# Kernel optimization log

Hardware: AMD Instinct MI355X
Metric: run time of the kernel (lower is better)

## Reference

```python
import jax, jax.numpy as jnp
import numpy as np

LN_EPS = 1e-12

def setup_inputs() -> dict:
    key = jax.random.key(0)
    k1, k2 = jax.random.split(key)
    B, S, H = 32, 2048, 1024
    input_tensor = jax.random.normal(k1, (B, S, H), dtype=jnp.float32)
    # learned params
    complex_weight = jax.random.normal(k2, (1, S // 2 + 1, H, 2), dtype=jnp.float32) * 0.02
    ln_gamma = jnp.ones((H,), dtype=jnp.float32)
    ln_beta = jnp.zeros((H,), dtype=jnp.float32)
    return {"input_tensor": input_tensor, "complex_weight": complex_weight,
            "ln_gamma": ln_gamma, "ln_beta": ln_beta}

def reference(input_tensor, complex_weight, ln_gamma, ln_beta):
    B, S, H = input_tensor.shape
    # FFT filter: rfft along seq, complex elementwise multiply, irfft
    x = jnp.fft.rfft(input_tensor, axis=1, norm='ortho')            # [B, S//2+1, H] complex64
    weight = complex_weight[..., 0] + 1j * complex_weight[..., 1]   # [1, S//2+1, H]
    x = x * weight
    seq_fft = jnp.fft.irfft(x, n=S, axis=1, norm='ortho')           # [B, S, H] real
    # dropout is identity in eval mode
    h = seq_fft + input_tensor
    # LayerNorm over last dim, eps=1e-12, biased variance (torch semantics)
    mean = jnp.mean(h, axis=-1, keepdims=True)
    var = jnp.mean(jnp.square(h - mean), axis=-1, keepdims=True)
    normed = (h - mean) * jax.lax.rsqrt(var + LN_EPS)
    return normed * ln_gamma + ln_beta
```

## Files before the change

kernel.cpp:

```cpp
#include <hip/hip_runtime.h>
#include <math.h>


#define PI_F 3.14159265358979323846f
#define SW(c) ((c) ^ (((c) >> 4) & 15))

__device__ __forceinline__ float2 cadd(float2 a, float2 b){ return make_float2(a.x+b.x, a.y+b.y); }
__device__ __forceinline__ float2 csub(float2 a, float2 b){ return make_float2(a.x-b.x, a.y-b.y); }
__device__ __forceinline__ float2 cmul(float2 a, float2 b){ return make_float2(a.x*b.x - a.y*b.y, a.x*b.y + a.y*b.x); }

template<int L>
__device__ __forceinline__ void fwd_stage(float2* A, int j){
  constexpr int half = L >> 1;
  const float ang0 = -PI_F / (float)L;
  #pragma unroll
  for (int r = 0; r < 4; ++r){
    int g    = j + (r << 7);
    int blk  = g / half;
    int joff = g - blk * half;
    int i0   = blk * (2 * L) + joff;
    float2 u0 = A[SW(i0)];
    float2 u1 = A[SW(i0 + half)];
    float2 u2 = A[SW(i0 + L)];
    float2 u3 = A[SW(i0 + L + half)];
    float sn, cs; __sincosf(ang0 * (float)joff, &sn, &cs);
    float2 w1 = make_float2(cs, sn);
    float2 t0  = cadd(u0, u2);
    float2 d02 = csub(u0, u2);
    float2 t1  = cadd(u1, u3);
    float2 d13 = csub(u1, u3);
    float2 t2  = cmul(d02, w1);
    float2 tm  = cmul(d13, w1);
    float2 t3  = make_float2(tm.y, -tm.x);
    float2 w2  = cmul(w1, w1);
    A[SW(i0)]            = cadd(t0, t1);
    A[SW(i0 + half)]     = cmul(csub(t0, t1), w2);
    A[SW(i0 + L)]        = cadd(t2, t3);
    A[SW(i0 + L + half)] = cmul(csub(t2, t3), w2);
  }
}

template<int l>
__device__ __forceinline__ void inv_stage(float2* A, int j){
  const float angB = PI_F / (float)(2 * l);
  #pragma unroll
  for (int r = 0; r < 4; ++r){
    int g    = j + (r << 7);
    int blk  = g / l;
    int joff = g - blk * l;
    int base = blk * (4 * l);
    int i0 = base + joff;
    float2 u0 = A[SW(i0)];
    float2 u1 = A[SW(i0 + l)];
    float2 u2 = A[SW(i0 + 2*l)];
    float2 u3 = A[SW(i0 + 3*l)];
    float sn, cs; __sincosf(angB * (float)joff, &sn, &cs);
    float2 wB = make_float2(cs, sn);
    float2 w  = cmul(wB, wB);
    float2 a1 = cmul(u1, w);
    float2 b0 = cadd(u0, a1), b1 = csub(u0, a1);
    float2 a3 = cmul(u3, w);
    float2 b2 = cadd(u2, a3), b3 = csub(u2, a3);
    float2 t2 = cmul(b2, wB);
    float2 c0 = cadd(b0, t2), c2 = csub(b0, t2);
    float2 iwB = make_float2(-wB.y, wB.x);
    float2 t3 = cmul(b3, iwB);
    float2 c1 = cadd(b1, t3), c3 = csub(b1, t3);
    A[SW(i0)]       = c0;
    A[SW(i0 + l)]   = c1;
    A[SW(i0 + 2*l)] = c2;
    A[SW(i0 + 3*l)] = c3;
  }
}

__device__ __forceinline__ float2 fetchW(const float2* __restrict__ wT,
                                         const float2* __restrict__ cw,
                                         int useT, int h, int k){
  if (useT) return wT[(size_t)h * 1025 + k];
  float2 w = cw[(size_t)k * 1024 + h];
  const float inv = 1.0f / 2048.0f;
  return make_float2((w.x + 1.0f) * inv, w.y * inv);
}

__global__ void prep_w_kernel(const float2* __restrict__ cw, float2* __restrict__ wT){
  __shared__ float2 tile[32][33];
  int k0 = blockIdx.x * 32, h0 = blockIdx.y * 32;
  int tx = threadIdx.x, ty = threadIdx.y;
  #pragma unroll
  for (int r = 0; r < 4; ++r){
    int k = k0 + ty + 8 * r;
    if (k < 1025) tile[ty + 8*r][tx] = cw[(size_t)k * 1024 + (h0 + tx)];
  }
  __syncthreads();
  const float inv = 1.0f / 2048.0f;
  #pragma unroll
  for (int r = 0; r < 4; ++r){
    int h = h0 + ty + 8 * r;
    int k = k0 + tx;
    if (k < 1025){
      float2 w = tile[tx][ty + 8*r];
      wT[(size_t)h * 1025 + k] = make_float2((w.x + 1.0f) * inv, w.y * inv);
    }
  }
}

__global__ __launch_bounds__(512) void fft_filter_kernel(
    const float2* __restrict__ x,
    const float2* __restrict__ cw,
    const float2* __restrict__ wT,
    int useT,
    float2* __restrict__ out){
  __shared__ float2 lds[4][2048];
  const int t  = threadIdx.x;
  const int bx = blockIdx.x;
  const int b  = bx >> 7;
  const int pg = bx & 127;
  const int f  = t >> 7;
  const int j  = t & 127;
  float2* A = lds[f];

  {
    const int p4 = t & 3, srow = t >> 2;
    const size_t base = ((size_t)b * 2048) * 512 + (size_t)(pg * 4 + p4);
    #pragma unroll
    for (int it = 0; it < 16; ++it){
      int s = srow + (it << 7);
      lds[p4][SW(s)] = x[base + (size_t)s * 512];
    }
  }
  __syncthreads();

  fwd_stage<1024>(A, j); __syncthreads();
  fwd_stage<256>(A, j);  __syncthreads();
  fwd_stage<64>(A, j);   __syncthreads();
  fwd_stage<16>(A, j);   __syncthreads();
  fwd_stage<4>(A, j);    __syncthreads();
  #pragma unroll
  for (int r = 0; r < 8; ++r){
    int m = j + (r << 7);
    int ia = SW(2*m), ib = SW(2*m + 1);
    float2 u = A[ia], v = A[ib];
    A[ia] = cadd(u, v);
    A[ib] = csub(u, v);
  }
  __syncthreads();

  {
    const int hA = (pg << 3) + (f << 1);
    if (j == 0){
      float2 z0 = A[0];
      float2 wa = fetchW(wT, cw, useT, hA, 0);
      float2 wb = fetchW(wT, cw, useT, hA + 1, 0);
      A[0] = make_float2(z0.x * wa.x, z0.y * wb.x);
      int p1 = SW(1);
      float2 zn = A[p1];
      wa = fetchW(wT, cw, useT, hA, 1024);
      wb = fetchW(wT, cw, useT, hA + 1, 1024);
      A[p1] = make_float2(zn.x * wa.x, zn.y * wb.x);
    }
    #pragma unroll
    for (int r = 0; r < 8; ++r){
      int k = 1 + j + (r << 7);
      if (k < 1024){
        int kr = 2048 - k;
        int p1 = SW((int)(__brev((unsigned)k) >> 21));
        int p2 = SW((int)(__brev((unsigned)kr) >> 21));
        float2 Z1 = A[p1], Z2 = A[p2];
        float2 Xa = make_float2(0.5f*(Z1.x + Z2.x), 0.5f*(Z1.y - Z2.y));
        float2 Xb = make_float2(0.5f*(Z1.y + Z2.y), 0.5f*(Z2.x - Z1.x));
        float2 wa = fetchW(wT, cw, useT, hA, k);
        float2 wb = fetchW(wT, cw, useT, hA + 1, k);
        float2 Ya = cmul(Xa, wa);
        float2 Yb = cmul(Xb, wb);
        A[p1] = make_float2(Ya.x - Yb.y, Ya.y + Yb.x);
        A[p2] = make_float2(Ya.x + Yb.y, Yb.x - Ya.y);
      }
    }
  }
  __syncthreads();

  #pragma unroll
  for (int r = 0; r < 8; ++r){
    int m = j + (r << 7);
    int ia = SW(2*m), ib = SW(2*m + 1);
    float2 u = A[ia], v = A[ib];
    A[ia] = cadd(u, v);
    A[ib] = csub(u, v);
  }
  __syncthreads();
  inv_stage<2>(A, j);   __syncthreads();
  inv_stage<8>(A, j);   __syncthreads();
  inv_stage<32>(A, j);  __syncthreads();
  inv_stage<128>(A, j); __syncthreads();
  inv_stage<512>(A, j); __syncthreads();

  {
    const int p4 = t & 3, srow = t >> 2;
    const size_t base = ((size_t)b * 2048) * 512 + (size_t)(pg * 4 + p4);
    #pragma unroll
    for (int it = 0; it < 16; ++it){
      int s = srow + (it << 7);
      out[base + (size_t)s * 512] = lds[p4][SW(s)];
    }
  }
}

__global__ __launch_bounds__(256) void ln_kernel(float* __restrict__ io,
                                                 const float* __restrict__ gma,
                                                 const float* __restrict__ bta){
  const int row = blockIdx.x;
  const int t = threadIdx.x;
  float4* r4 = (float4*)io + (size_t)row * 256;
  float4 v = r4[t];
  float s1 = v.x + v.y + v.z + v.w;
  float s2 = v.x*v.x + v.y*v.y + v.z*v.z + v.w*v.w;
  #pragma unroll
  for (int off = 32; off > 0; off >>= 1){
    s1 += __shfl_down(s1, off);
    s2 += __shfl_down(s2, off);
  }
  __shared__ float red[8];
  __shared__ float mr[2];
  const int wid = t >> 6, lane = t & 63;
  if (lane == 0){ red[wid] = s1; red[4 + wid] = s2; }
  __syncthreads();
  if (t == 0){
    float ts1 = red[0] + red[1] + red[2] + red[3];
    float ts2 = red[4] + red[5] + red[6] + red[7];
    float mean = ts1 * (1.0f / 1024.0f);
    float var  = ts2 * (1.0f / 1024.0f) - mean * mean;
    mr[0] = mean;
    mr[1] = rsqrtf(fmaxf(var, 0.0f) + 1e-12f);
  }
  __syncthreads();
  const float mean = mr[0], rstd = mr[1];
  const float4 gv = ((const float4*)gma)[t];
  const float4 bv = ((const float4*)bta)[t];
  float4 o;
  o.x = (v.x - mean) * rstd * gv.x + bv.x;
  o.y = (v.y - mean) * rstd * gv.y + bv.y;
  o.z = (v.z - mean) * rstd * gv.z + bv.z;
  o.w = (v.w - mean) * rstd * gv.w + bv.w;
  r4[t] = o;
}

extern "C" void kernel_launch(void* const* d_in, const int* in_sizes, int n_in,
                              void* d_out, int out_size, void* d_ws, size_t ws_size,
                              hipStream_t stream){
  const float2* x2  = (const float2*)d_in[0];
  const float2* cw2 = (const float2*)d_in[1];
  const float*  gma = (const float*)d_in[2];
  const float*  bta = (const float*)d_in[3];
  float2* out2 = (float2*)d_out;
  float*  outf = (float*)d_out;

  const int Bn = in_sizes[0] / (2048 * 1024);

  const size_t needW = (size_t)1025 * 1024 * sizeof(float2);
  const int useT = (ws_size >= needW) ? 1 : 0;
  float2* wT = (float2*)d_ws;

  if (useT){
    hipLaunchKernelGGL(prep_w_kernel, dim3(33, 32), dim3(32, 8), 0, stream, cw2, wT);
  }
  hipLaunchKernelGGL(fft_filter_kernel, dim3(Bn * 128), dim3(512), 0, stream,
                     x2, cw2, wT, useT, out2);
  hipLaunchKernelGGL(ln_kernel, dim3(Bn * 2048), dim3(256), 0, stream,
                     outf, gma, bta);
}
```

Measured before the change: 891.6 us.

## Replace radix-4 LDS FFT stages with register radix-16 plus shuffle stages

Result: slower. 1.635 ms (+83.4%).

```diff
diff --git a/kernel.cpp b/kernel.cpp
--- a/kernel.cpp
+++ b/kernel.cpp
@@ -2,75 +2,61 @@
 #include <math.h>
 
 
-#define PI_F 3.14159265358979323846f
-#define SW(c) ((c) ^ (((c) >> 4) & 15))
+#define C8f  0.70710678118654752f
+#define SIN1 0.38268343236508977f
+#define COS1 0.92387953251128674f
+
+#define SW4(i) ((i) ^ ((((i) >> 8) & 7) << 3))
+
+static constexpr int BR4[16] = {0,8,4,12,2,10,6,14,1,9,5,13,3,11,7,15};
 
 __device__ __forceinline__ float2 cadd(float2 a, float2 b){ return make_float2(a.x+b.x, a.y+b.y); }
 __device__ __forceinline__ float2 csub(float2 a, float2 b){ return make_float2(a.x-b.x, a.y-b.y); }
 __device__ __forceinline__ float2 cmul(float2 a, float2 b){ return make_float2(a.x*b.x - a.y*b.y, a.x*b.y + a.y*b.x); }
 
-template<int L>
-__device__ __forceinline__ void fwd_stage(float2* A, int j){
-  constexpr int half = L >> 1;
-  const float ang0 = -PI_F / (float)L;
-  #pragma unroll
-  for (int r = 0; r < 4; ++r){
-    int g    = j + (r << 7);
-    int blk  = g / half;
-    int joff = g - blk * half;
-    int i0   = blk * (2 * L) + joff;
-    float2 u0 = A[SW(i0)];
-    float2 u1 = A[SW(i0 + half)];
-    float2 u2 = A[SW(i0 + L)];
-    float2 u3 = A[SW(i0 + L + half)];
-    float sn, cs; __sincosf(ang0 * (float)joff, &sn, &cs);
-    float2 w1 = make_float2(cs, sn);
-    float2 t0  = cadd(u0, u2);
-    float2 d02 = csub(u0, u2);
-    float2 t1  = cadd(u1, u3);
-    float2 d13 = csub(u1, u3);
-    float2 t2  = cmul(d02, w1);
-    float2 tm  = cmul(d13, w1);
-    float2 t3  = make_float2(tm.y, -tm.x);
-    float2 w2  = cmul(w1, w1);
-    A[SW(i0)]            = cadd(t0, t1);
-    A[SW(i0 + half)]     = cmul(csub(t0, t1), w2);
-    A[SW(i0 + L)]        = cadd(t2, t3);
-    A[SW(i0 + L + half)] = cmul(csub(t2, t3), w2);
-  }
-}
-
-template<int l>
-__device__ __forceinline__ void inv_stage(float2* A, int j){
-  const float angB = PI_F / (float)(2 * l);
-  #pragma unroll
-  for (int r = 0; r < 4; ++r){
-    int g    = j + (r << 7);
-    int blk  = g / l;
-    int joff = g - blk * l;
-    int base = blk * (4 * l);
-    int i0 = base + joff;
-    float2 u0 = A[SW(i0)];
-    float2 u1 = A[SW(i0 + l)];
-    float2 u2 = A[SW(i0 + 2*l)];
-    float2 u3 = A[SW(i0 + 3*l)];
-    float sn, cs; __sincosf(angB * (float)joff, &sn, &cs);
-    float2 wB = make_float2(cs, sn);
-    float2 w  = cmul(wB, wB);
-    float2 a1 = cmul(u1, w);
-    float2 b0 = cadd(u0, a1), b1 = csub(u0, a1);
-    float2 a3 = cmul(u3, w);
-    float2 b2 = cadd(u2, a3), b3 = csub(u2, a3);
-    float2 t2 = cmul(b2, wB);
-    float2 c0 = cadd(b0, t2), c2 = csub(b0, t2);
-    float2 iwB = make_float2(-wB.y, wB.x);
-    float2 t3 = cmul(b3, iwB);
-    float2 c1 = cadd(b1, t3), c3 = csub(b1, t3);
-    A[SW(i0)]       = c0;
-    A[SW(i0 + l)]   = c1;
-    A[SW(i0 + 2*l)] = c2;
-    A[SW(i0 + 3*l)] = c3;
-  }
+__device__ __forceinline__ void dft16_fwd(float2* r){
+  const float WR[8] = {1.f,  COS1,  C8f,  SIN1, 0.f, -SIN1, -C8f, -COS1};
+  const float WI[8] = {0.f, -SIN1, -C8f, -COS1, -1.f, -COS1, -C8f, -SIN1};
+  #pragma unroll
+  for (int m = 0; m < 8; ++m){
+    float2 u = r[m], v = r[m+8];
+    r[m] = cadd(u, v);
+    float2 d = csub(u, v);
+    r[m+8] = make_float2(d.x*WR[m] - d.y*WI[m], d.x*WI[m] + d.y*WR[m]);
+  }
+  #pragma unroll
+  for (int h = 0; h < 16; h += 8){
+    #pragma unroll
+    for (int m = 0; m < 4; ++m){
+      float2 u = r[h+m], v = r[h+m+4];
+      r[h+m] = cadd(u, v);
+      float2 d = csub(u, v);
+      r[h+m+4] = make_float2(d.x*WR[2*m] - d.y*WI[2*m], d.x*WI[2*m] + d.y*WR[2*m]);
+    }
+  }
+  #pragma unroll
+  for (int h = 0; h < 16; h += 4){
+    { float2 u=r[h],   v=r[h+2]; r[h]  =cadd(u,v); r[h+2]=csub(u,v); }
+    { float2 u=r[h+1], v=r[h+3]; float2 d=csub(u,v); r[h+1]=cadd(u,v); r[h+3]=make_float2(d.y, -d.x); }
+  }
+  #pragma unroll
+  for (int h = 0; h < 16; h += 2){
+    float2 u=r[h], v=r[h+1]; r[h]=cadd(u,v); r[h+1]=csub(u,v);
+  }
+}
+
+__device__ __forceinline__ void twiddle_apply(float2* r, float2 step){
+  float2 tw = step;
+  #pragma unroll
+  for (int k = 1; k < 16; ++k){
+    int p = BR4[k];
+    r[p] = cmul(r[p], tw);
+    if (k < 15) tw = cmul(tw, step);
+  }
+}
+
+__device__ __forceinline__ float2 shflx(float2 v, int m){
+  return make_float2(__shfl_xor(v.x, m, 64), __shfl_xor(v.y, m, 64));
 }
 
 __device__ __forceinline__ float2 fetchW(const float2* __restrict__ wT,
@@ -104,7 +90,7 @@
   }
 }
 
-__global__ __launch_bounds__(512) void fft_filter_kernel(
+__global__ __launch_bounds__(512, 4) void fft_filter_kernel(
     const float2* __restrict__ x,
     const float2* __restrict__ cw,
     const float2* __restrict__ wT,
@@ -125,74 +111,130 @@
     #pragma unroll
     for (int it = 0; it < 16; ++it){
       int s = srow + (it << 7);
-      lds[p4][SW(s)] = x[base + (size_t)s * 512];
-    }
-  }
-  __syncthreads();
-
-  fwd_stage<1024>(A, j); __syncthreads();
-  fwd_stage<256>(A, j);  __syncthreads();
-  fwd_stage<64>(A, j);   __syncthreads();
-  fwd_stage<16>(A, j);   __syncthreads();
-  fwd_stage<4>(A, j);    __syncthreads();
-  #pragma unroll
-  for (int r = 0; r < 8; ++r){
-    int m = j + (r << 7);
-    int ia = SW(2*m), ib = SW(2*m + 1);
-    float2 u = A[ia], v = A[ib];
-    A[ia] = cadd(u, v);
-    A[ib] = csub(u, v);
-  }
-  __syncthreads();
-
-  {
-    const int hA = (pg << 3) + (f << 1);
-    if (j == 0){
-      float2 z0 = A[0];
+      lds[p4][SW4(s)] = x[base + (size_t)s * 512];
+    }
+  }
+  __syncthreads();
+
+  float2 r[16];
+  const int k1 = j >> 3, bb = j & 7;
+  const int rb = ((bb & 1) << 2) | (bb & 2) | ((bb & 4) >> 2);
+
+  const float2 w8c = make_float2((bb & 1) ? ((bb & 2) ? -C8f : C8f) : ((bb & 2) ? 0.f : 1.f),
+                                 (bb & 1) ? -C8f : ((bb & 2) ? -1.f : 0.f));
+  const float2 w4c = (bb & 1) ? make_float2(0.f, -1.f) : make_float2(1.f, 0.f);
+  const bool h4 = (bb & 4), h2 = (bb & 2), h1 = (bb & 1);
+
+  float sn, cs;
+  __sincosf(-6.2831853071795864769f * (float)j * (1.0f / 2048.0f), &sn, &cs);
+  const float2 stepJ = make_float2(cs, sn);
+  __sincosf(-6.2831853071795864769f * (float)bb * (1.0f / 128.0f), &sn, &cs);
+  const float2 stepB = make_float2(cs, sn);
+
+  #pragma unroll
+  for (int n1 = 0; n1 < 16; ++n1) r[n1] = A[SW4(128 * n1 + j)];
+  dft16_fwd(r);
+  twiddle_apply(r, stepJ);
+  __syncthreads();
+  #pragma unroll
+  for (int p = 0; p < 16; ++p){
+    int kk1 = BR4[p];
+    A[128 * kk1 + (j ^ ((kk1 & 1) << 3))] = r[p];
+  }
+  __syncthreads();
+
+  #pragma unroll
+  for (int a = 0; a < 16; ++a)
+    r[a] = A[128 * k1 + (((a << 3) + bb) ^ ((k1 & 1) << 3))];
+  dft16_fwd(r);
+  twiddle_apply(r, stepB);
+
+  #pragma unroll
+  for (int p = 0; p < 16; ++p){
+    float2 z = r[p];
+    float2 tt = shflx(z, 4);
+    float2 a1 = h4 ? csub(tt, z) : cadd(z, tt);
+    z = h4 ? cmul(a1, w8c) : a1;
+    tt = shflx(z, 2);
+    a1 = h2 ? csub(tt, z) : cadd(z, tt);
+    z = h2 ? cmul(a1, w4c) : a1;
+    tt = shflx(z, 1);
+    r[p] = h1 ? csub(tt, z) : cadd(z, tt);
+  }
+  __syncthreads();
+  #pragma unroll
+  for (int p = 0; p < 16; ++p){
+    int c = BR4[p];
+    int k = k1 + (c << 4) + (rb << 8);
+    A[SW4(k)] = r[p];
+  }
+  __syncthreads();
+
+  const int hA = (pg << 3) + (f << 1);
+  #pragma unroll
+  for (int q = 0; q < 16; ++q){
+    int kk = (q << 7) + j;
+    float2 V;
+    if (kk == 0){
+      float2 X0 = A[SW4(0)];
       float2 wa = fetchW(wT, cw, useT, hA, 0);
       float2 wb = fetchW(wT, cw, useT, hA + 1, 0);
-      A[0] = make_float2(z0.x * wa.x, z0.y * wb.x);
-      int p1 = SW(1);
-      float2 zn = A[p1];
-      wa = fetchW(wT, cw, useT, hA, 1024);
-      wb = fetchW(wT, cw, useT, hA + 1, 1024);
-      A[p1] = make_float2(zn.x * wa.x, zn.y * wb.x);
-    }
-    #pragma unroll
-    for (int r = 0; r < 8; ++r){
-      int k = 1 + j + (r << 7);
-      if (k < 1024){
-        int kr = 2048 - k;
-        int p1 = SW((int)(__brev((unsigned)k) >> 21));
-        int p2 = SW((int)(__brev((unsigned)kr) >> 21));
-        float2 Z1 = A[p1], Z2 = A[p2];
-        float2 Xa = make_float2(0.5f*(Z1.x + Z2.x), 0.5f*(Z1.y - Z2.y));
-        float2 Xb = make_float2(0.5f*(Z1.y + Z2.y), 0.5f*(Z2.x - Z1.x));
-        float2 wa = fetchW(wT, cw, useT, hA, k);
-        float2 wb = fetchW(wT, cw, useT, hA + 1, k);
-        float2 Ya = cmul(Xa, wa);
-        float2 Yb = cmul(Xb, wb);
-        A[p1] = make_float2(Ya.x - Yb.y, Ya.y + Yb.x);
-        A[p2] = make_float2(Ya.x + Yb.y, Yb.x - Ya.y);
-      }
-    }
-  }
-  __syncthreads();
-
-  #pragma unroll
-  for (int r = 0; r < 8; ++r){
-    int m = j + (r << 7);
-    int ia = SW(2*m), ib = SW(2*m + 1);
-    float2 u = A[ia], v = A[ib];
-    A[ia] = cadd(u, v);
-    A[ib] = csub(u, v);
-  }
-  __syncthreads();
-  inv_stage<2>(A, j);   __syncthreads();
-  inv_stage<8>(A, j);   __syncthreads();
-  inv_stage<32>(A, j);  __syncthreads();
-  inv_stage<128>(A, j); __syncthreads();
-  inv_stage<512>(A, j); __syncthreads();
+      V = make_float2(X0.x * wa.x, X0.y * wb.x);
+    } else if (kk == 1024){
+      float2 Xn = A[SW4(1024)];
+      float2 wa = fetchW(wT, cw, useT, hA, 1024);
+      float2 wb = fetchW(wT, cw, useT, hA + 1, 1024);
+      V = make_float2(Xn.x * wa.x, Xn.y * wb.x);
+    } else {
+      int k = (kk < 1024) ? kk : 2048 - kk;
+      float2 Z1 = A[SW4(k)];
+      float2 Z2 = A[SW4(2048 - k)];
+      float2 wa = fetchW(wT, cw, useT, hA, k);
+      float2 wb = fetchW(wT, cw, useT, hA + 1, k);
+      float2 Xa = make_float2(0.5f*(Z1.x + Z2.x), 0.5f*(Z1.y - Z2.y));
+      float2 Xb = make_float2(0.5f*(Z1.y + Z2.y), 0.5f*(Z2.x - Z1.x));
+      float2 Ya = cmul(Xa, wa);
+      float2 Yb = cmul(Xb, wb);
+      V = (kk < 1024) ? make_float2(Ya.x - Yb.y, Ya.y + Yb.x)
+                      : make_float2(Ya.x + Yb.y, Yb.x - Ya.y);
+    }
+    r[q] = make_float2(V.x, -V.y);
+  }
+
+  dft16_fwd(r);
+  twiddle_apply(r, stepJ);
+  __syncthreads();
+  #pragma unroll
+  for (int p = 0; p < 16; ++p){
+    int s1 = BR4[p];
+    A[128 * s1 + (j ^ ((s1 & 1) << 3))] = r[p];
+  }
+  __syncthreads();
+  #pragma unroll
+  for (int a = 0; a < 16; ++a)
+    r[a] = A[128 * k1 + (((a << 3) + bb) ^ ((k1 & 1) << 3))];
+  dft16_fwd(r);
+  twiddle_apply(r, stepB);
+  #pragma unroll
+  for (int p = 0; p < 16; ++p){
+    float2 z = r[p];
+    float2 tt = shflx(z, 4);
+    float2 a1 = h4 ? csub(tt, z) : cadd(z, tt);
+    z = h4 ? cmul(a1, w8c) : a1;
+    tt = shflx(z, 2);
+    a1 = h2 ? csub(tt, z) : cadd(z, tt);
+    z = h2 ? cmul(a1, w4c) : a1;
+    tt = shflx(z, 1);
+    r[p] = h1 ? csub(tt, z) : cadd(z, tt);
+  }
+  __syncthreads();
+  #pragma unroll
+  for (int p = 0; p < 16; ++p){
+    int g = BR4[p];
+    int s = k1 + (g << 4) + (rb << 8);
+    A[SW4(s)] = make_float2(r[p].x, -r[p].y);
+  }
+  __syncthreads();
 
   {
     const int p4 = t & 3, srow = t >> 2;
@@ -200,7 +242,7 @@
     #pragma unroll
     for (int it = 0; it < 16; ++it){
       int s = srow + (it << 7);
-      out[base + (size_t)s * 512] = lds[p4][SW(s)];
+      out[base + (size_t)s * 512] = lds[p4][SW4(s)];
     }
   }
 }
@@ -208,40 +250,38 @@
 __global__ __launch_bounds__(256) void ln_kernel(float* __restrict__ io,
                                                  const float* __restrict__ gma,
                                                  const float* __restrict__ bta){
-  const int row = blockIdx.x;
   const int t = threadIdx.x;
-  float4* r4 = (float4*)io + (size_t)row * 256;
-  float4 v = r4[t];
-  float s1 = v.x + v.y + v.z + v.w;
-  float s2 = v.x*v.x + v.y*v.y + v.z*v.z + v.w*v.w;
-  #pragma unroll
-  for (int off = 32; off > 0; off >>= 1){
-    s1 += __shfl_down(s1, off);
-    s2 += __shfl_down(s2, off);
-  }
-  __shared__ float red[8];
-  __shared__ float mr[2];
-  const int wid = t >> 6, lane = t & 63;
-  if (lane == 0){ red[wid] = s1; red[4 + wid] = s2; }
-  __syncthreads();
-  if (t == 0){
-    float ts1 = red[0] + red[1] + red[2] + red[3];
-    float ts2 = red[4] + red[5] + red[6] + red[7];
-    float mean = ts1 * (1.0f / 1024.0f);
-    float var  = ts2 * (1.0f / 1024.0f) - mean * mean;
-    mr[0] = mean;
-    mr[1] = rsqrtf(fmaxf(var, 0.0f) + 1e-12f);
-  }
-  __syncthreads();
-  const float mean = mr[0], rstd = mr[1];
-  const float4 gv = ((const float4*)gma)[t];
-  const float4 bv = ((const float4*)bta)[t];
-  float4 o;
-  o.x = (v.x - mean) * rstd * gv.x + bv.x;
-  o.y = (v.y - mean) * rstd * gv.y + bv.y;
-  o.z = (v.z - mean) * rstd * gv.z + bv.z;
-  o.w = (v.w - mean) * rstd * gv.w + bv.w;
-  r4[t] = o;
+  const int lane = t & 63;
+  const size_t row = (size_t)blockIdx.x * 4 + (t >> 6);
+  float4* r4 = (float4*)io + row * 256;
+  const float4* g4 = (const float4*)gma;
+  const float4* b4 = (const float4*)bta;
+  float4 v[4];
+  #pragma unroll
+  for (int i = 0; i < 4; ++i) v[i] = r4[lane + 64 * i];
+  float s1 = 0.f, s2 = 0.f;
+  #pragma unroll
+  for (int i = 0; i < 4; ++i){
+    s1 += v[i].x + v[i].y + v[i].z + v[i].w;
+    s2 += v[i].x*v[i].x + v[i].y*v[i].y + v[i].z*v[i].z + v[i].w*v[i].w;
+  }
+  #pragma unroll
+  for (int m = 32; m >= 1; m >>= 1){
+    s1 += __shfl_xor(s1, m, 64);
+    s2 += __shfl_xor(s2, m, 64);
+  }
+  const float mean = s1 * (1.0f / 1024.0f);
+  const float var  = s2 * (1.0f / 1024.0f) - mean * mean;
+  const float rstd = rsqrtf(fmaxf(var, 0.0f) + 1e-12f);
+  #pragma unroll
+  for (int i = 0; i < 4; ++i){
+    float4 gv = g4[lane + 64 * i], bv = b4[lane + 64 * i], o;
+    o.x = (v[i].x - mean) * rstd * gv.x + bv.x;
+    o.y = (v[i].y - mean) * rstd * gv.y + bv.y;
+    o.z = (v[i].z - mean) * rstd * gv.z + bv.z;
+    o.w = (v[i].w - mean) * rstd * gv.w + bv.w;
+    r4[lane + 64 * i] = o;
+  }
 }
 
 extern "C" void kernel_launch(void* const* d_in, const int* in_sizes, int n_in,
@@ -265,6 +305,6 @@
   }
   hipLaunchKernelGGL(fft_filter_kernel, dim3(Bn * 128), dim3(512), 0, stream,
                      x2, cw2, wT, useT, out2);
-  hipLaunchKernelGGL(ln_kernel, dim3(Bn * 2048), dim3(256), 0, stream,
+  hipLaunchKernelGGL(ln_kernel, dim3(Bn * 512), dim3(256), 0, stream,
                      outf, gma, bta);
 }
```
